# Optimization experiments

Measured on AMD Instinct MI355X. Metric: run time of the kernel, lower is better.

Reference implementation:

```python
import jax, jax.numpy as jnp
import numpy as np

N_NODES, N_VARS, E = 100000, 50000, 640000
FEAT, H, L = 16, 128, 4
N_INT, K = 20000, 8  # integer vars with categorical heads, uniform domain size


def _mlp2(x, W1, b1, W2, b2):
    return jnp.maximum(x @ W1 + b1, 0.0) @ W2 + b2


def setup_inputs() -> dict:
    key = jax.random.key(0)
    ks = jax.random.split(key, 24)
    s = lambda i, shape, scale: jax.random.normal(ks[i], shape, dtype=jnp.float32) * scale
    inp = {
        "x": jax.random.normal(ks[0], (N_NODES, FEAT), dtype=jnp.float32),
        "edge_index": jax.random.randint(ks[1], (2, E), 0, N_NODES, dtype=jnp.int32).astype(jnp.int64),
        "num_vars": N_VARS,
        # NodeEmbedder (var / cons)
        "ve_W1": s(2, (FEAT, H), 0.25), "ve_b1": jnp.zeros((H,), jnp.float32),
        "ve_W2": s(3, (H, H), 0.09),   "ve_b2": jnp.zeros((H,), jnp.float32),
        "ce_W1": s(4, (FEAT, H), 0.25), "ce_b1": jnp.zeros((H,), jnp.float32),
        "ce_W2": s(5, (H, H), 0.09),   "ce_b2": jnp.zeros((H,), jnp.float32),
        # GCN backbone: stacked per-layer params
        "conv_W": s(6, (L, H, H), 0.09), "conv_b": jnp.zeros((L, H), jnp.float32),
        "ref_W1": s(7, (L, H, H), 0.09), "ref_b1": jnp.zeros((L, H), jnp.float32),
        "ref_W2": s(8, (L, H, H), 0.09), "ref_b2": jnp.zeros((L, H), jnp.float32),
        # Bernoulli head: H -> H//2 -> 1
        "bh_W1": s(9, (H, H // 2), 0.09), "bh_b1": jnp.zeros((H // 2,), jnp.float32),
        "bh_W2": s(10, (H // 2, 1), 0.12), "bh_b2": jnp.zeros((1,), jnp.float32),
        # Categorical heads: one Linear(H, K) per integer variable, batched
        "cat_W": s(11, (N_INT, H, K), 0.09),
        "cat_b": jnp.zeros((N_INT, K), jnp.float32),
    }
    return inp


def reference(x, edge_index, num_vars,
              ve_W1, ve_b1, ve_W2, ve_b2,
              ce_W1, ce_b1, ce_W2, ce_b2,
              conv_W, conv_b, ref_W1, ref_b1, ref_W2, ref_b2,
              bh_W1, bh_b1, bh_W2, bh_b2,
              cat_W, cat_b):
    N = x.shape[0]
    src, dst = edge_index[0], edge_index[1]
    # GCN normalization with self-loops: deg includes the self edge
    deg = jax.ops.segment_sum(jnp.ones((src.shape[0],), x.dtype), dst, num_segments=N) + 1.0
    dinv_sqrt = jax.lax.rsqrt(deg)
    enorm = dinv_sqrt[src] * dinv_sqrt[dst]      # [E]
    self_norm = (1.0 / deg)[:, None]             # [N,1] self-loop weight deg^-1

    var_h = _mlp2(x[:num_vars], ve_W1, ve_b1, ve_W2, ve_b2)
    cons_h = _mlp2(x[num_vars:], ce_W1, ce_b1, ce_W2, ce_b2)
    h = jnp.concatenate([var_h, cons_h], axis=0)  # [N,H]

    def gcn_conv(xin, W, b):
        hw = xin @ W
        agg = jax.ops.segment_sum(hw[src] * enorm[:, None], dst, num_segments=N)
        return agg + hw * self_norm + b

    def layer(xc, p):
        W, b, W1, b1, W2, b2 = p
        h_ = jnp.maximum(gcn_conv(xc, W, b), 0.0)
        return xc + _mlp2(h_, W1, b1, W2, b2), None

    h, _ = jax.lax.scan(layer, h, (conv_W, conv_b, ref_W1, ref_b1, ref_W2, ref_b2))

    vh = h[:num_vars]
    bern_logits = _mlp2(vh, bh_W1, bh_b1, bh_W2, bh_b2)[:, 0]          # [num_vars]
    n_int = cat_W.shape[0]
    cat_logits = jnp.einsum('nh,nhk->nk', vh[:n_int], cat_W) + cat_b    # [n_int,K]
    return bern_logits, cat_logits
```

## Files before the change

kernel.cpp:

```cpp
#include <hip/hip_runtime.h>
#include <hip/hip_bf16.h>

#define NN 100000
#define NV 50000
#define NE 640000
#define FEAT 16
#define HD 128
#define NL 4
#define NI 20000
#define KK 8
#define SCAN_BLK 98
#define LDP 136
#define WE_STRIDE (128*32 + 128*128)

typedef __hip_bfloat16 bf16;
typedef __attribute__((ext_vector_type(8))) short short8;
typedef __attribute__((ext_vector_type(4))) float f32x4;

static __device__ __forceinline__ ushort f2bu(float f) {
    __hip_bfloat16 b = __float2bfloat16(f);
    return *reinterpret_cast<ushort*>(&b);
}
static __device__ __forceinline__ float bu2f(ushort u) {
    __hip_bfloat16 b = *reinterpret_cast<__hip_bfloat16*>(&u);
    return __bfloat162float(b);
}

__global__ void k_deg_init(float* deg) {
    int i = blockIdx.x * blockDim.x + threadIdx.x;
    if (i < NN) deg[i] = 1.0f;
}

__global__ void k_deg_scatter(const int* __restrict__ ei, float* deg) {
    int e = blockIdx.x * blockDim.x + threadIdx.x;
    if (e < NE) atomicAdd(&deg[ei[NE + e]], 1.0f);
}

__global__ void k_deg_fin(const float* __restrict__ deg, float* dinv, float* selfn) {
    int i = blockIdx.x * blockDim.x + threadIdx.x;
    if (i < NN) {
        float d = deg[i];
        dinv[i]  = rsqrtf(d);
        selfn[i] = 1.0f / d;
    }
}

__global__ void k_scan_part(const float* __restrict__ deg, int* __restrict__ part) {
    __shared__ int s[256];
    const int t = threadIdx.x;
    const int i = blockIdx.x * 1024 + t * 4;
    int sum = 0;
#pragma unroll
    for (int j = 0; j < 4; ++j)
        if (i + j < NN) sum += (int)deg[i + j] - 1;
    s[t] = sum;
    __syncthreads();
    for (int off = 128; off > 0; off >>= 1) {
        if (t < off) s[t] += s[t + off];
        __syncthreads();
    }
    if (t == 0) part[blockIdx.x] = s[0];
}

__global__ void k_scan_mid(const int* __restrict__ part, int* __restrict__ blockoff,
                           int* __restrict__ row_ptr) {
    __shared__ int s[128];
    const int t = threadIdx.x;
    int v = (t < SCAN_BLK) ? part[t] : 0;
    s[t] = v;
    __syncthreads();
    for (int off = 1; off < 128; off <<= 1) {
        int u = (t >= off) ? s[t - off] : 0;
        __syncthreads();
        s[t] += u;
        __syncthreads();
    }
    if (t < SCAN_BLK) blockoff[t] = s[t] - v;
    if (t == 0) row_ptr[NN] = NE;
}

__global__ void k_scan_apply(const float* __restrict__ deg,
                             const int* __restrict__ blockoff,
                             int* __restrict__ row_ptr, int* __restrict__ cnt) {
    __shared__ int s[256];
    const int t = threadIdx.x;
    const int i = blockIdx.x * 1024 + t * 4;
    int c[4];
    int tsum = 0;
#pragma unroll
    for (int j = 0; j < 4; ++j) {
        c[j] = (i + j < NN) ? (int)deg[i + j] - 1 : 0;
        tsum += c[j];
    }
    s[t] = tsum;
    __syncthreads();
    for (int off = 1; off < 256; off <<= 1) {
        int u = (t >= off) ? s[t - off] : 0;
        __syncthreads();
        s[t] += u;
        __syncthreads();
    }
    int off = blockoff[blockIdx.x] + s[t] - tsum;
#pragma unroll
    for (int j = 0; j < 4; ++j) {
        if (i + j < NN) {
            row_ptr[i + j] = off;
            cnt[i + j] = 0;
            off += c[j];
        }
    }
}

__global__ void k_csr_fill(const int* __restrict__ ei,
                           const int* __restrict__ row_ptr, int* __restrict__ cnt,
                           const float* __restrict__ dinv,
                           int* __restrict__ col, float* __restrict__ wgt) {
    int e = blockIdx.x * blockDim.x + threadIdx.x;
    if (e >= NE) return;
    const int s = ei[e];
    const int d = ei[NE + e];
    const int pos = row_ptr[d] + atomicAdd(&cnt[d], 1);
    col[pos] = s;
    wgt[pos] = dinv[s] * dinv[d];
}

__global__ void k_wprep(const float* __restrict__ conv_W,
                        const float* __restrict__ ref_W1,
                        const float* __restrict__ ref_W2,
                        ushort* __restrict__ wt) {
    const int mat = blockIdx.x >> 7;
    const int j = blockIdx.x & 127;
    const int k = threadIdx.x;
    const float* src = (mat < 4) ? conv_W + (size_t)mat * HD * HD
                     : (mat < 8) ? ref_W1 + (size_t)(mat - 4) * HD * HD
                                 : ref_W2 + (size_t)(mat - 8) * HD * HD;
    wt[(size_t)mat * HD * HD + j * HD + k] = f2bu(src[k * HD + j]);
}

__global__ void k_wprep_embed(const float* __restrict__ vW1, const float* __restrict__ vW2,
                              const float* __restrict__ cW1, const float* __restrict__ cW2,
                              ushort* __restrict__ wte) {
    const int side = blockIdx.x >> 7;
    const int j = blockIdx.x & 127;
    const int k = threadIdx.x;
    const float* W1 = side ? cW1 : vW1;
    const float* W2 = side ? cW2 : vW2;
    ushort* o = wte + (size_t)side * WE_STRIDE;
    if (k < 32) o[j * 32 + k] = (k < FEAT) ? f2bu(W1[k * HD + j]) : (ushort)0;
    o[128 * 32 + j * HD + k] = f2bu(W2[k * HD + j]);
}

__global__ __launch_bounds__(256, 4) void k_embed_mfma(
        const float* __restrict__ x,
        const ushort* __restrict__ W1t, const float* __restrict__ b1,
        const ushort* __restrict__ W2t, const float* __restrict__ b2,
        int nbase, int nend,
        ushort* __restrict__ hb) {
    const int lane = threadIdx.x & 63, w = threadIdx.x >> 6;
    const int l15 = lane & 15, lg = lane >> 4;
    const int rowb = nbase + blockIdx.x * 128;
    __shared__ ushort hsm[128][LDP];

#pragma unroll
    for (int rt = 0; rt < 2; ++rt) {
        const int r = rowb + w * 32 + rt * 16 + l15;
        const int rc = r < nend ? r : nend - 1;
        short8 a = {0, 0, 0, 0, 0, 0, 0, 0};
        if (lg < 2) {
            const float* xp = x + (size_t)rc * FEAT + lg * 8;
#pragma unroll
            for (int i = 0; i < 8; ++i) a[i] = (short)f2bu(xp[i]);
        }
#pragma unroll
        for (int jt = 0; jt < 8; ++jt) {
            const float bv = b1[jt * 16 + l15];
            f32x4 acc = {bv, bv, bv, bv};
            short8 b = *reinterpret_cast<const short8*>(&W1t[(jt * 16 + l15) * 32 + lg * 8]);
            acc = __builtin_amdgcn_mfma_f32_16x16x32_bf16(a, b, acc, 0, 0, 0);
#pragma unroll
            for (int rr = 0; rr < 4; ++rr)
                hsm[w * 32 + rt * 16 + lg * 4 + rr][jt * 16 + l15] =
                    f2bu(fmaxf(acc[rr], 0.0f));
        }
    }
    __syncthreads();

#pragma unroll
    for (int rt = 0; rt < 2; ++rt) {
        f32x4 acc[8];
#pragma unroll
        for (int jt = 0; jt < 8; ++jt) {
            const float bv = b2[jt * 16 + l15];
            f32x4 v = {bv, bv, bv, bv};
            acc[jt] = v;
        }
#pragma unroll
        for (int ks = 0; ks < 4; ++ks) {
            short8 a = *reinterpret_cast<const short8*>(&hsm[w * 32 + rt * 16 + l15][ks * 32 + lg * 8]);
#pragma unroll
            for (int jt = 0; jt < 8; ++jt) {
                short8 b = *reinterpret_cast<const short8*>(&W2t[(jt * 16 + l15) * HD + ks * 32 + lg * 8]);
                acc[jt] = __builtin_amdgcn_mfma_f32_16x16x32_bf16(a, b, acc[jt], 0, 0, 0);
            }
        }
#pragma unroll
        for (int jt = 0; jt < 8; ++jt)
#pragma unroll
            for (int rr = 0; rr < 4; ++rr) {
                const int row = rowb + w * 32 + rt * 16 + lg * 4 + rr;
                if (row < nend)
                    hb[(size_t)row * HD + jt * 16 + l15] = f2bu(acc[jt][rr]);
            }
    }
}

__global__ __launch_bounds__(256) void k_hw(
                     const ushort* __restrict__ hb, const ushort* __restrict__ Wt,
                     ushort* __restrict__ hwb) {
    const int lane = threadIdx.x & 63;
    const int w = threadIdx.x >> 6;
    const int row0 = blockIdx.x * 128 + w * 32;
    const int l15 = lane & 15, lg = lane >> 4;

    const f32x4 zero = {0.f, 0.f, 0.f, 0.f};
    f32x4 acc[2][8];
#pragma unroll
    for (int rt = 0; rt < 2; ++rt)
#pragma unroll
        for (int jt = 0; jt < 8; ++jt) acc[rt][jt] = zero;

#pragma unroll
    for (int ks = 0; ks < 4; ++ks) {
        short8 a[2];
#pragma unroll
        for (int rt = 0; rt < 2; ++rt) {
            int r = row0 + rt * 16 + l15;
            r = r < NN ? r : NN - 1;
            a[rt] = *reinterpret_cast<const short8*>(&hb[(size_t)r * HD + ks * 32 + lg * 8]);
        }
#pragma unroll
        for (int jt = 0; jt < 8; ++jt) {
            short8 b = *reinterpret_cast<const short8*>(&Wt[(jt * 16 + l15) * HD + ks * 32 + lg * 8]);
            acc[0][jt] = __builtin_amdgcn_mfma_f32_16x16x32_bf16(a[0], b, acc[0][jt], 0, 0, 0);
            acc[1][jt] = __builtin_amdgcn_mfma_f32_16x16x32_bf16(a[1], b, acc[1][jt], 0, 0, 0);
        }
    }
#pragma unroll
    for (int rt = 0; rt < 2; ++rt)
#pragma unroll
        for (int jt = 0; jt < 8; ++jt)
#pragma unroll
            for (int r = 0; r < 4; ++r) {
                int row = row0 + rt * 16 + lg * 4 + r;
                if (row < NN) hwb[(size_t)row * HD + jt * 16 + l15] = f2bu(acc[rt][jt][r]);
            }
}

__global__ __launch_bounds__(512, 4) void k_combine(
                          const ushort* __restrict__ hwb,
                          const int* __restrict__ row_ptr,
                          const int* __restrict__ col,
                          const float* __restrict__ wgt,
                          const float* __restrict__ selfn,
                          const float* __restrict__ cb,
                          const ushort* __restrict__ Wt1, const float* __restrict__ b1,
                          const ushort* __restrict__ Wt2, const float* __restrict__ b2,
                          ushort* __restrict__ hb) {
    const int t = threadIdx.x;
    const int n0 = blockIdx.x * 64;
    __shared__ ushort hs[64][LDP];
    __shared__ ushort hid[64][LDP];
    __shared__ int rp[65];

    if (t <= 64) {
        int idx = n0 + t;
        rp[t] = row_ptr[idx < NN ? idx : NN];
    }
    __syncthreads();

    const int lane = t & 63, w = t >> 6;
    {
        const int c0 = 2 * lane;
        const float cbx = cb[c0], cby = cb[c0 + 1];
        float accx[8], accy[8];
        int ecur[8], eend[8];
        int rounds = 0;
#pragma unroll
        for (int m = 0; m < 8; ++m) {
            const int node = n0 + w * 8 + m;
            const int nc = node < NN ? node : NN - 1;
            const uint hv = *reinterpret_cast<const uint*>(&hwb[(size_t)nc * HD + c0]);
            const float sn = selfn[nc];
            accx[m] = bu2f((ushort)(hv & 0xffffu)) * sn + cbx;
            accy[m] = bu2f((ushort)(hv >> 16)) * sn + cby;
            ecur[m] = rp[w * 8 + m];
            eend[m] = rp[w * 8 + m + 1];
            rounds = max(rounds, eend[m] - ecur[m]);
        }
#pragma unroll 1
        for (int r = 0; r < rounds; r += 2) {
            uint va[8], vb[8];
            float wa[8], wb[8];
            int ca[8], cc[8];
#pragma unroll
            for (int m = 0; m < 8; ++m) {
                const int e0 = ecur[m];
                const int a0 = (e0 < eend[m]) ? e0 : 0;
                const int a1 = (e0 + 1 < eend[m]) ? e0 + 1 : 0;
                wa[m] = (e0 < eend[m]) ? wgt[a0] : 0.0f;
                wb[m] = (e0 + 1 < eend[m]) ? wgt[a1] : 0.0f;
                ca[m] = col[a0];
                cc[m] = col[a1];
            }
#pragma unroll
            for (int m = 0; m < 8; ++m) {
                va[m] = *reinterpret_cast<const uint*>(&hwb[(size_t)ca[m] * HD + c0]);
                vb[m] = *reinterpret_cast<const uint*>(&hwb[(size_t)cc[m] * HD + c0]);
            }
#pragma unroll
            for (int m = 0; m < 8; ++m) {
                accx[m] += wa[m] * bu2f((ushort)(va[m] & 0xffffu));
                accy[m] += wa[m] * bu2f((ushort)(va[m] >> 16));
                accx[m] += wb[m] * bu2f((ushort)(vb[m] & 0xffffu));
                accy[m] += wb[m] * bu2f((ushort)(vb[m] >> 16));
            }
#pragma unroll
            for (int m = 0; m < 8; ++m) ecur[m] += 2;
        }
#pragma unroll
        for (int m = 0; m < 8; ++m) {
            const uint px = (uint)f2bu(fmaxf(accx[m], 0.0f));
            const uint py = (uint)f2bu(fmaxf(accy[m], 0.0f));
            *reinterpret_cast<uint*>(&hs[w * 8 + m][c0]) = px | (py << 16);
        }
    }
    __syncthreads();

    const int l15 = lane & 15, lg = lane >> 4;
    const int rt = (w & 3) * 16;
    const int c0 = (w >> 2) * 64;

    f32x4 acc1[4];
#pragma unroll
    for (int jt = 0; jt < 4; ++jt) {
        float bv = b1[c0 + jt * 16 + l15];
        f32x4 v = {bv, bv, bv, bv};
        acc1[jt] = v;
    }
#pragma unroll
    for (int ks = 0; ks < 4; ++ks) {
        short8 a = *reinterpret_cast<const short8*>(&hs[rt + l15][ks * 32 + lg * 8]);
#pragma unroll
        for (int jt = 0; jt < 4; ++jt) {
            short8 b = *reinterpret_cast<const short8*>(&Wt1[(c0 + jt * 16 + l15) * HD + ks * 32 + lg * 8]);
            acc1[jt] = __builtin_amdgcn_mfma_f32_16x16x32_bf16(a, b, acc1[jt], 0, 0, 0);
        }
    }
#pragma unroll
    for (int jt = 0; jt < 4; ++jt)
#pragma unroll
        for (int r = 0; r < 4; ++r)
            hid[rt + lg * 4 + r][c0 + jt * 16 + l15] = f2bu(fmaxf(acc1[jt][r], 0.0f));
    __syncthreads();

    f32x4 acc2[4];
#pragma unroll
    for (int jt = 0; jt < 4; ++jt) {
        float bv = b2[c0 + jt * 16 + l15];
        f32x4 v = {bv, bv, bv, bv};
        acc2[jt] = v;
    }
#pragma unroll
    for (int ks = 0; ks < 4; ++ks) {
        short8 a = *reinterpret_cast<const short8*>(&hid[rt + l15][ks * 32 + lg * 8]);
#pragma unroll
        for (int jt = 0; jt < 4; ++jt) {
            short8 b = *reinterpret_cast<const short8*>(&Wt2[(c0 + jt * 16 + l15) * HD + ks * 32 + lg * 8]);
            acc2[jt] = __builtin_amdgcn_mfma_f32_16x16x32_bf16(a, b, acc2[jt], 0, 0, 0);
        }
    }
#pragma unroll
    for (int jt = 0; jt < 4; ++jt)
#pragma unroll
        for (int r = 0; r < 4; ++r) {
            const int row = n0 + rt + lg * 4 + r;
            if (row < NN) {
                const size_t idx = (size_t)row * HD + c0 + jt * 16 + l15;
                hb[idx] = f2bu(acc2[jt][r] + bu2f(hb[idx]));
            }
        }
}

__global__ void k_bern(const ushort* __restrict__ hb,
                       const float* __restrict__ W1, const float* __restrict__ b1,
                       const float* __restrict__ W2, const float* __restrict__ b2,
                       float* __restrict__ out) {
    const long long t = (long long)blockIdx.x * blockDim.x + threadIdx.x;
    const int n = (int)(t >> 6);
    const int lane = (int)(t & 63);
    if (n >= NV) return;
    const ushort* hn = hb + (size_t)n * HD;
    float acc = b1[lane];
#pragma unroll 8
    for (int k = 0; k < HD; ++k) acc += bu2f(hn[k]) * W1[k * 64 + lane];
    float p = fmaxf(acc, 0.0f) * W2[lane];
#pragma unroll
    for (int off = 32; off > 0; off >>= 1) p += __shfl_down(p, off);
    if (lane == 0) out[n] = p + b2[0];
}

__global__ void k_cat(const ushort* __restrict__ hb,
                      const float* __restrict__ cW, const float* __restrict__ cb,
                      float* __restrict__ out) {
    const long long t = (long long)blockIdx.x * blockDim.x + threadIdx.x;
    const int n = (int)(t >> 6);
    const int lane = (int)(t & 63);
    if (n >= NI) return;
    const ushort* hn = hb + (size_t)n * HD;
    float p[KK];
#pragma unroll
    for (int k = 0; k < KK; ++k) p[k] = 0.0f;
#pragma unroll
    for (int half = 0; half < 2; ++half) {
        const int hh = lane + 64 * half;
        const float vh = bu2f(hn[hh]);
        const float* wp = cW + ((size_t)n * HD + hh) * KK;
#pragma unroll
        for (int k = 0; k < KK; ++k) p[k] += vh * wp[k];
    }
#pragma unroll
    for (int k = 0; k < KK; ++k) {
#pragma unroll
        for (int off = 32; off > 0; off >>= 1) p[k] += __shfl_down(p[k], off);
    }
    if (lane == 0) {
#pragma unroll
        for (int k = 0; k < KK; ++k) out[NV + (size_t)n * KK + k] = p[k] + cb[(size_t)n * KK + k];
    }
}

extern "C" void kernel_launch(void* const* d_in, const int* in_sizes, int n_in,
                              void* d_out, int out_size, void* d_ws, size_t ws_size,
                              hipStream_t stream) {
    const float* x  = (const float*)d_in[0];
    const int*   ei = (const int*)d_in[1];
    const float* ve_W1 = (const float*)d_in[3];
    const float* ve_b1 = (const float*)d_in[4];
    const float* ve_W2 = (const float*)d_in[5];
    const float* ve_b2 = (const float*)d_in[6];
    const float* ce_W1 = (const float*)d_in[7];
    const float* ce_b1 = (const float*)d_in[8];
    const float* ce_W2 = (const float*)d_in[9];
    const float* ce_b2 = (const float*)d_in[10];
    const float* conv_W = (const float*)d_in[11];
    const float* conv_b = (const float*)d_in[12];
    const float* ref_W1 = (const float*)d_in[13];
    const float* ref_b1 = (const float*)d_in[14];
    const float* ref_W2 = (const float*)d_in[15];
    const float* ref_b2 = (const float*)d_in[16];
    const float* bh_W1 = (const float*)d_in[17];
    const float* bh_b1 = (const float*)d_in[18];
    const float* bh_W2 = (const float*)d_in[19];
    const float* bh_b2 = (const float*)d_in[20];
    const float* cat_W = (const float*)d_in[21];
    const float* cat_b = (const float*)d_in[22];
    float* out = (float*)d_out;

    const size_t need = (size_t)(3 * NN + (NN + 1) + NN + 2 * NE + 2 * SCAN_BLK) * 4
                      + (size_t)NN * HD * 2
                      + (size_t)NN * HD * 2
                      + (size_t)12 * HD * HD * 2
                      + (size_t)2 * WE_STRIDE * 2;
    if (ws_size < need) return;

    float* deg     = (float*)d_ws;
    float* dinv    = deg + NN;
    float* selfn   = dinv + NN;
    int*   row_ptr = (int*)(selfn + NN);
    int*   cnt     = row_ptr + (NN + 1);
    int*   col     = cnt + NN;
    float* wgt     = (float*)(col + NE);
    int*   part    = (int*)(wgt + NE);
    int*   blockoff= part + SCAN_BLK;
    ushort* hwb    = (ushort*)(blockoff + SCAN_BLK);
    ushort* hb     = hwb + (size_t)NN * HD;
    ushort* wt     = hb + (size_t)NN * HD;
    ushort* wte    = wt + (size_t)12 * HD * HD;

    k_deg_init<<<(NN + 255) / 256, 256, 0, stream>>>(deg);
    k_deg_scatter<<<(NE + 255) / 256, 256, 0, stream>>>(ei, deg);
    k_deg_fin<<<(NN + 255) / 256, 256, 0, stream>>>(deg, dinv, selfn);
    k_scan_part<<<SCAN_BLK, 256, 0, stream>>>(deg, part);
    k_scan_mid<<<1, 128, 0, stream>>>(part, blockoff, row_ptr);
    k_scan_apply<<<SCAN_BLK, 256, 0, stream>>>(deg, blockoff, row_ptr, cnt);
    k_csr_fill<<<(NE + 255) / 256, 256, 0, stream>>>(ei, row_ptr, cnt, dinv, col, wgt);
    k_wprep<<<12 * 128, 128, 0, stream>>>(conv_W, ref_W1, ref_W2, wt);
    k_wprep_embed<<<256, 128, 0, stream>>>(ve_W1, ve_W2, ce_W1, ce_W2, wte);

    k_embed_mfma<<<(NV + 127) / 128, 256, 0, stream>>>(
        x, wte, ve_b1, wte + 128 * 32, ve_b2, 0, NV, hb);
    k_embed_mfma<<<(NN - NV + 127) / 128, 256, 0, stream>>>(
        x, wte + WE_STRIDE, ce_b1, wte + WE_STRIDE + 128 * 32, ce_b2, NV, NN, hb);

    for (int l = 0; l < NL; ++l) {
        k_hw<<<(NN + 127) / 128, 256, 0, stream>>>(hb, wt + (size_t)l * HD * HD, hwb);
        k_combine<<<(NN + 63) / 64, 512, 0, stream>>>(hwb, row_ptr, col, wgt, selfn,
                                               conv_b + (size_t)l * HD,
                                               wt + (size_t)(4 + l) * HD * HD,
                                               ref_b1 + (size_t)l * HD,
                                               wt + (size_t)(8 + l) * HD * HD,
                                               ref_b2 + (size_t)l * HD,
                                               hb);
    }

    k_bern<<<(NV * 64) / 256, 256, 0, stream>>>(hb, bh_W1, bh_b1, bh_W2, bh_b2, out);
    k_cat<<<(NI * 64) / 256, 256, 0, stream>>>(hb, cat_W, cat_b, out);
}
```

Measured before the change: 769.4 us.

## Fuse next-layer GCN weight matmul into embed and combine kernels

Removes the separate k_hw kernel. The next layer's h@W_conv is now computed inside the embedding kernel and at the tail of each combine kernel, using the freshly produced rows already held in LDS. hw is ping-ponged between two workspace buffers so the gather source for one layer is not overwritten by the next. The hid LDS buffer is dropped in favour of reusing hs, which adds extra syncs and raises register pressure in the fused kernels. The categorical head's weight loads are also vectorised to float4.

Result: slower. 792.9 us (+3.1%).

```diff
diff --git a/kernel.cpp b/kernel.cpp
--- a/kernel.cpp
+++ b/kernel.cpp
@@ -1,5 +1,6 @@
 #include <hip/hip_runtime.h>
 #include <hip/hip_bf16.h>
+
 
 #define NN 100000
 #define NV 50000
@@ -154,8 +155,9 @@
         const float* __restrict__ x,
         const ushort* __restrict__ W1t, const float* __restrict__ b1,
         const ushort* __restrict__ W2t, const float* __restrict__ b2,
+        const ushort* __restrict__ Wtc,
         int nbase, int nend,
-        ushort* __restrict__ hb) {
+        ushort* __restrict__ hb, ushort* __restrict__ hwb) {
     const int lane = threadIdx.x & 63, w = threadIdx.x >> 6;
     const int l15 = lane & 15, lg = lane >> 4;
     const int rowb = nbase + blockIdx.x * 128;
@@ -208,52 +210,32 @@
 #pragma unroll
             for (int rr = 0; rr < 4; ++rr) {
                 const int row = rowb + w * 32 + rt * 16 + lg * 4 + rr;
+                const ushort hv = f2bu(acc[jt][rr]);
+                if (row < nend) hb[(size_t)row * HD + jt * 16 + l15] = hv;
+                hsm[w * 32 + rt * 16 + lg * 4 + rr][jt * 16 + l15] = hv;
+            }
+        f32x4 acc3[8];
+        const f32x4 zero = {0.f, 0.f, 0.f, 0.f};
+#pragma unroll
+        for (int jt = 0; jt < 8; ++jt) acc3[jt] = zero;
+#pragma unroll
+        for (int ks = 0; ks < 4; ++ks) {
+            short8 a = *reinterpret_cast<const short8*>(&hsm[w * 32 + rt * 16 + l15][ks * 32 + lg * 8]);
+#pragma unroll
+            for (int jt = 0; jt < 8; ++jt) {
+                short8 b = *reinterpret_cast<const short8*>(&Wtc[(jt * 16 + l15) * HD + ks * 32 + lg * 8]);
+                acc3[jt] = __builtin_amdgcn_mfma_f32_16x16x32_bf16(a, b, acc3[jt], 0, 0, 0);
+            }
+        }
+#pragma unroll
+        for (int jt = 0; jt < 8; ++jt)
+#pragma unroll
+            for (int rr = 0; rr < 4; ++rr) {
+                const int row = rowb + w * 32 + rt * 16 + lg * 4 + rr;
                 if (row < nend)
-                    hb[(size_t)row * HD + jt * 16 + l15] = f2bu(acc[jt][rr]);
-            }
-    }
-}
-
-__global__ __launch_bounds__(256) void k_hw(
-                     const ushort* __restrict__ hb, const ushort* __restrict__ Wt,
-                     ushort* __restrict__ hwb) {
-    const int lane = threadIdx.x & 63;
-    const int w = threadIdx.x >> 6;
-    const int row0 = blockIdx.x * 128 + w * 32;
-    const int l15 = lane & 15, lg = lane >> 4;
-
-    const f32x4 zero = {0.f, 0.f, 0.f, 0.f};
-    f32x4 acc[2][8];
-#pragma unroll
-    for (int rt = 0; rt < 2; ++rt)
-#pragma unroll
-        for (int jt = 0; jt < 8; ++jt) acc[rt][jt] = zero;
-
-#pragma unroll
-    for (int ks = 0; ks < 4; ++ks) {
-        short8 a[2];
-#pragma unroll
-        for (int rt = 0; rt < 2; ++rt) {
-            int r = row0 + rt * 16 + l15;
-            r = r < NN ? r : NN - 1;
-            a[rt] = *reinterpret_cast<const short8*>(&hb[(size_t)r * HD + ks * 32 + lg * 8]);
-        }
-#pragma unroll
-        for (int jt = 0; jt < 8; ++jt) {
-            short8 b = *reinterpret_cast<const short8*>(&Wt[(jt * 16 + l15) * HD + ks * 32 + lg * 8]);
-            acc[0][jt] = __builtin_amdgcn_mfma_f32_16x16x32_bf16(a[0], b, acc[0][jt], 0, 0, 0);
-            acc[1][jt] = __builtin_amdgcn_mfma_f32_16x16x32_bf16(a[1], b, acc[1][jt], 0, 0, 0);
-        }
-    }
-#pragma unroll
-    for (int rt = 0; rt < 2; ++rt)
-#pragma unroll
-        for (int jt = 0; jt < 8; ++jt)
-#pragma unroll
-            for (int r = 0; r < 4; ++r) {
-                int row = row0 + rt * 16 + lg * 4 + r;
-                if (row < NN) hwb[(size_t)row * HD + jt * 16 + l15] = f2bu(acc[rt][jt][r]);
-            }
+                    hwb[(size_t)row * HD + jt * 16 + l15] = f2bu(acc3[jt][rr]);
+            }
+    }
 }
 
 __global__ __launch_bounds__(512, 4) void k_combine(
@@ -265,11 +247,12 @@
                           const float* __restrict__ cb,
                           const ushort* __restrict__ Wt1, const float* __restrict__ b1,
                           const ushort* __restrict__ Wt2, const float* __restrict__ b2,
-                          ushort* __restrict__ hb) {
+                          ushort* __restrict__ hb,
+                          const ushort* __restrict__ Wtc, ushort* __restrict__ hwb_out,
+                          int do_hw) {
     const int t = threadIdx.x;
     const int n0 = blockIdx.x * 64;
     __shared__ ushort hs[64][LDP];
-    __shared__ ushort hid[64][LDP];
     __shared__ int rp[65];
 
     if (t <= 64) {
@@ -356,11 +339,12 @@
             acc1[jt] = __builtin_amdgcn_mfma_f32_16x16x32_bf16(a, b, acc1[jt], 0, 0, 0);
         }
     }
+    __syncthreads();
 #pragma unroll
     for (int jt = 0; jt < 4; ++jt)
 #pragma unroll
         for (int r = 0; r < 4; ++r)
-            hid[rt + lg * 4 + r][c0 + jt * 16 + l15] = f2bu(fmaxf(acc1[jt][r], 0.0f));
+            hs[rt + lg * 4 + r][c0 + jt * 16 + l15] = f2bu(fmaxf(acc1[jt][r], 0.0f));
     __syncthreads();
 
     f32x4 acc2[4];
@@ -372,22 +356,56 @@
     }
 #pragma unroll
     for (int ks = 0; ks < 4; ++ks) {
-        short8 a = *reinterpret_cast<const short8*>(&hid[rt + l15][ks * 32 + lg * 8]);
+        short8 a = *reinterpret_cast<const short8*>(&hs[rt + l15][ks * 32 + lg * 8]);
 #pragma unroll
         for (int jt = 0; jt < 4; ++jt) {
             short8 b = *reinterpret_cast<const short8*>(&Wt2[(c0 + jt * 16 + l15) * HD + ks * 32 + lg * 8]);
             acc2[jt] = __builtin_amdgcn_mfma_f32_16x16x32_bf16(a, b, acc2[jt], 0, 0, 0);
         }
     }
+    ushort hnew[4][4];
 #pragma unroll
     for (int jt = 0; jt < 4; ++jt)
 #pragma unroll
         for (int r = 0; r < 4; ++r) {
             const int row = n0 + rt + lg * 4 + r;
-            if (row < NN) {
-                const size_t idx = (size_t)row * HD + c0 + jt * 16 + l15;
-                hb[idx] = f2bu(acc2[jt][r] + bu2f(hb[idx]));
-            }
+            const int rc = row < NN ? row : NN - 1;
+            const size_t idx = (size_t)rc * HD + c0 + jt * 16 + l15;
+            const ushort hv = f2bu(acc2[jt][r] + bu2f(hb[idx]));
+            hnew[jt][r] = hv;
+            if (row < NN) hb[idx] = hv;
+        }
+
+    if (!do_hw) return;
+
+    __syncthreads();
+#pragma unroll
+    for (int jt = 0; jt < 4; ++jt)
+#pragma unroll
+        for (int r = 0; r < 4; ++r)
+            hs[rt + lg * 4 + r][c0 + jt * 16 + l15] = hnew[jt][r];
+    __syncthreads();
+
+    f32x4 acc3[4];
+    const f32x4 zero = {0.f, 0.f, 0.f, 0.f};
+#pragma unroll
+    for (int jt = 0; jt < 4; ++jt) acc3[jt] = zero;
+#pragma unroll
+    for (int ks = 0; ks < 4; ++ks) {
+        short8 a = *reinterpret_cast<const short8*>(&hs[rt + l15][ks * 32 + lg * 8]);
+#pragma unroll
+        for (int jt = 0; jt < 4; ++jt) {
+            short8 b = *reinterpret_cast<const short8*>(&Wtc[(c0 + jt * 16 + l15) * HD + ks * 32 + lg * 8]);
+            acc3[jt] = __builtin_amdgcn_mfma_f32_16x16x32_bf16(a, b, acc3[jt], 0, 0, 0);
+        }
+    }
+#pragma unroll
+    for (int jt = 0; jt < 4; ++jt)
+#pragma unroll
+        for (int r = 0; r < 4; ++r) {
+            const int row = n0 + rt + lg * 4 + r;
+            if (row < NN)
+                hwb_out[(size_t)row * HD + c0 + jt * 16 + l15] = f2bu(acc3[jt][r]);
         }
 }
 
@@ -425,8 +443,10 @@
         const int hh = lane + 64 * half;
         const float vh = bu2f(hn[hh]);
         const float* wp = cW + ((size_t)n * HD + hh) * KK;
-#pragma unroll
-        for (int k = 0; k < KK; ++k) p[k] += vh * wp[k];
+        const float4 w0 = *reinterpret_cast<const float4*>(wp);
+        const float4 w1 = *reinterpret_cast<const float4*>(wp + 4);
+        p[0] += vh * w0.x; p[1] += vh * w0.y; p[2] += vh * w0.z; p[3] += vh * w0.w;
+        p[4] += vh * w1.x; p[5] += vh * w1.y; p[6] += vh * w1.z; p[7] += vh * w1.w;
     }
 #pragma unroll
     for (int k = 0; k < KK; ++k) {
@@ -467,8 +487,7 @@
     float* out = (float*)d_out;
 
     const size_t need = (size_t)(3 * NN + (NN + 1) + NN + 2 * NE + 2 * SCAN_BLK) * 4
-                      + (size_t)NN * HD * 2
-                      + (size_t)NN * HD * 2
+                      + (size_t)3 * NN * HD * 2
                       + (size_t)12 * HD * HD * 2
                       + (size_t)2 * WE_STRIDE * 2;
     if (ws_size < need) return;
@@ -482,8 +501,9 @@
     float* wgt     = (float*)(col + NE);
     int*   part    = (int*)(wgt + NE);
     int*   blockoff= part + SCAN_BLK;
-    ushort* hwb    = (ushort*)(blockoff + SCAN_BLK);
-    ushort* hb     = hwb + (size_t)NN * HD;
+    ushort* hwbA   = (ushort*)(blockoff + SCAN_BLK);
+    ushort* hwbB   = hwbA + (size_t)NN * HD;
+    ushort* hb     = hwbB + (size_t)NN * HD;
     ushort* wt     = hb + (size_t)NN * HD;
     ushort* wte    = wt + (size_t)12 * HD * HD;
 
@@ -498,19 +518,22 @@
     k_wprep_embed<<<256, 128, 0, stream>>>(ve_W1, ve_W2, ce_W1, ce_W2, wte);
 
     k_embed_mfma<<<(NV + 127) / 128, 256, 0, stream>>>(
-        x, wte, ve_b1, wte + 128 * 32, ve_b2, 0, NV, hb);
+        x, wte, ve_b1, wte + 128 * 32, ve_b2, wt, 0, NV, hb, hwbA);
     k_embed_mfma<<<(NN - NV + 127) / 128, 256, 0, stream>>>(
-        x, wte + WE_STRIDE, ce_b1, wte + WE_STRIDE + 128 * 32, ce_b2, NV, NN, hb);
+        x, wte + WE_STRIDE, ce_b1, wte + WE_STRIDE + 128 * 32, ce_b2, wt, NV, NN, hb, hwbA);
 
     for (int l = 0; l < NL; ++l) {
-        k_hw<<<(NN + 127) / 128, 256, 0, stream>>>(hb, wt + (size_t)l * HD * HD, hwb);
-        k_combine<<<(NN + 63) / 64, 512, 0, stream>>>(hwb, row_ptr, col, wgt, selfn,
+        ushort* hin  = (l & 1) ? hwbB : hwbA;
+        ushort* hout = (l & 1) ? hwbA : hwbB;
+        k_combine<<<(NN + 63) / 64, 512, 0, stream>>>(hin, row_ptr, col, wgt, selfn,
                                                conv_b + (size_t)l * HD,
                                                wt + (size_t)(4 + l) * HD * HD,
                                                ref_b1 + (size_t)l * HD,
                                                wt + (size_t)(8 + l) * HD * HD,
                                                ref_b2 + (size_t)l * HD,
-                                               hb);
+                                               hb,
+                                               wt + (size_t)(l + 1) * HD * HD,
+                                               hout, l < NL - 1 ? 1 : 0);
     }
 
     k_bern<<<(NV * 64) / 256, 256, 0, stream>>>(hb, bh_W1, bh_b1, bh_W2, bh_b2, out);
```
